# Kernel tuning notes

Hardware: AMD Instinct MI355X
Metric: run time of the kernel (lower is better)

The kernel has to match this reference:

```python
import jax, jax.numpy as jnp
import numpy as np

EMBED_DIM = 512
NUM_HEADS = 8
HEAD_DIM = EMBED_DIM // NUM_HEADS
EDGE_HIDDEN = 512
B, L = 2, 512


def setup_inputs() -> dict:
    key = jax.random.key(0)
    ks = jax.random.split(key, 16)
    s = 0.02
    inp = {
        "query": jax.random.normal(ks[0], (B, L, EMBED_DIM), jnp.float32),
        "key_in": jax.random.normal(ks[1], (B, L, EMBED_DIM), jnp.float32),
        "value": jax.random.normal(ks[2], (B, L, EMBED_DIM), jnp.float32),
        "edge_representation": jax.random.normal(ks[3], (B, L, L), jnp.float32),
        # projection weights stored as [in, out]: y = x @ W + b
        "Wq": jax.random.normal(ks[4], (EMBED_DIM, EMBED_DIM), jnp.float32) * s,
        "bq": jnp.zeros((EMBED_DIM,), jnp.float32),
        "Wk": jax.random.normal(ks[5], (EMBED_DIM, EMBED_DIM), jnp.float32) * s,
        "bk": jnp.zeros((EMBED_DIM,), jnp.float32),
        "Wv": jax.random.normal(ks[6], (EMBED_DIM, EMBED_DIM), jnp.float32) * s,
        "bv": jnp.zeros((EMBED_DIM,), jnp.float32),
        "Wo": jax.random.normal(ks[7], (EMBED_DIM, EMBED_DIM), jnp.float32) * s,
        "bo": jnp.zeros((EMBED_DIM,), jnp.float32),
        # edge MLP: Linear(1 -> 512) -> ReLU -> Linear(512 -> num_heads)
        "We1": jax.random.normal(ks[8], (1, EDGE_HIDDEN), jnp.float32) * s,
        "be1": jnp.zeros((EDGE_HIDDEN,), jnp.float32),
        "We2": jax.random.normal(ks[9], (EDGE_HIDDEN, NUM_HEADS), jnp.float32) * s,
        "be2": jnp.zeros((NUM_HEADS,), jnp.float32),
    }
    return inp


def reference(query, key_in, value, edge_representation,
              Wq, bq, Wk, bk, Wv, bv, Wo, bo, We1, be1, We2, be2):
    Bc, Lc, _ = query.shape
    # project and split heads: [B, H, L, Dh]
    def split_heads(x):
        return x.reshape(Bc, Lc, NUM_HEADS, HEAD_DIM).transpose(0, 2, 1, 3)
    Q = split_heads(query @ Wq + bq)
    K = split_heads(key_in @ Wk + bk)
    V = split_heads(value @ Wv + bv)
    # edge MLP on scalar edge features: [B, L, L, 1] -> [B, L, L, H]
    e = edge_representation[..., None]
    h = jax.nn.relu(e * We1[0] + be1)          # [B, L, L, 512]
    edge_bias = h @ We2 + be2                   # [B, L, L, H]
    scale = 1.0 / jnp.sqrt(jnp.asarray(HEAD_DIM, query.dtype))
    scores = jnp.einsum("bhqd,bhkd->bhqk", Q, K) * scale
    scores = scores + edge_bias.transpose(0, 3, 1, 2)  # [B, H, L, L]
    attn = jax.nn.softmax(scores, axis=-1)
    out = jnp.einsum("bhqk,bhkd->bhqd", attn, V)
    out = out.transpose(0, 2, 1, 3).reshape(Bc, Lc, EMBED_DIM)
    return out @ Wo + bo
```

## Files before the change

kernel.cpp:

```cpp
#include <hip/hip_runtime.h>
#include <hip/hip_bf16.h>

typedef __attribute__((ext_vector_type(8))) short bf16x8;
typedef __attribute__((ext_vector_type(4))) float f32x4;

#define LOG2E 1.44269504088896340736f

#define XQ_OFF 0
#define XK_OFF 524288
#define XV_OFF 1048576
#define WQ_OFF 1572864
#define WK_OFF 1835008
#define WV_OFF 2097152
#define WO_OFF 2359296
#define QB_OFF 2621440
#define KB_OFF 3145728
#define VT_OFF 3670016
#define AO_OFF 4194304
#define T_B   9437184
#define A_B   (T_B + 4096)
#define C_B   (A_B + 20480)
#define SEG_B (C_B + 20480)

struct MegaArgs {
  const float *xq, *xk, *xv, *eg;
  const float *wq, *wk, *wv, *wo;
  const float *bq, *bk, *bv, *bo;
  const float *w1, *b1, *we2, *be2;
  float* out;
  unsigned short* wsb;
  float *wsT, *wsA, *wsC;
  unsigned short* segp;
};

__device__ __forceinline__ unsigned short f2bf(float f) {
  union { __hip_bfloat16 h; unsigned short u; } c;
  c.h = __float2bfloat16(f);
  return c.u;
}

__device__ void prep_block(const MegaArgs& a, char* smem) {
  float* sT   = (float*)smem;
  int*   sIdx = (int*)(smem + 2048);
  float (*sDA)[8] = (float (*)[8])(smem + 4096);
  float (*sDC)[8] = (float (*)[8])(smem + 20480);
  float* sA0 = (float*)(smem + 36864);
  float* sC0 = (float*)(smem + 36896);
  int tid = threadIdx.x;
  for (int p = tid; p < 512; p += 256) {
    float w = a.w1[p], bb = a.b1[p];
    sT[p] = (w != 0.f) ? (-bb / w) : -3.4e38f;
    sIdx[p] = p;
#pragma unroll
    for (int h = 0; h < 8; ++h) {
      float w2 = a.we2[p * 8 + h];
      float ra = 0.f, rc = 0.f;
      if (w < 0.f)       { ra = w2 * w; rc = w2 * bb; }
      else if (w == 0.f) { rc = w2 * fmaxf(bb, 0.f); }
      sDA[p][h] = ra; sDC[p][h] = rc;
    }
  }
  __syncthreads();
  for (int size = 2; size <= 512; size <<= 1) {
    for (int stride = size >> 1; stride > 0; stride >>= 1) {
      int p = tid;
      int i = ((p / stride) * (stride << 1)) + (p % stride);
      int j = i + stride;
      bool up = ((i & size) == 0);
      float ti = sT[i], tj = sT[j];
      if (up ? (ti > tj) : (ti < tj)) {
        sT[i] = tj; sT[j] = ti;
        int t = sIdx[i]; sIdx[i] = sIdx[j]; sIdx[j] = t;
      }
      __syncthreads();
    }
  }
#pragma unroll
  for (int h = 0; h < 8; ++h) { sDA[tid][h] += sDA[tid + 256][h]; sDC[tid][h] += sDC[tid + 256][h]; }
  __syncthreads();
  for (int st = 128; st > 0; st >>= 1) {
    if (tid < st) {
#pragma unroll
      for (int h = 0; h < 8; ++h) { sDA[tid][h] += sDA[tid + st][h]; sDC[tid][h] += sDC[tid + st][h]; }
    }
    __syncthreads();
  }
  if (tid < 8) { sA0[tid] = sDA[0][tid]; sC0[tid] = sDC[0][tid] + a.be2[tid]; }
  __syncthreads();
  for (int p = tid; p < 512; p += 256) {
    int k = sIdx[p];
    float wk = a.w1[k], bk2 = a.b1[k];
#pragma unroll
    for (int h = 0; h < 8; ++h) {
      float w2 = a.we2[k * 8 + h];
      float da = 0.f, dc = 0.f;
      if (wk > 0.f)      { da =  w2 * wk; dc =  w2 * bk2; }
      else if (wk < 0.f) { da = -w2 * wk; dc = -w2 * bk2; }
      sDA[p][h] = da; sDC[p][h] = dc;
    }
  }
  __syncthreads();
  for (int off = 1; off < 512; off <<= 1) {
    float ra[2][8], rc[2][8];
#pragma unroll
    for (int e = 0; e < 2; ++e) {
      int p = tid + e * 256;
      if (p >= off) {
#pragma unroll
        for (int h = 0; h < 8; ++h) { ra[e][h] = sDA[p - off][h]; rc[e][h] = sDC[p - off][h]; }
      }
    }
    __syncthreads();
#pragma unroll
    for (int e = 0; e < 2; ++e) {
      int p = tid + e * 256;
      if (p >= off) {
#pragma unroll
        for (int h = 0; h < 8; ++h) { sDA[p][h] += ra[e][h]; sDC[p][h] += rc[e][h]; }
      }
    }
    __syncthreads();
  }
  a.wsT[tid] = sT[tid]; a.wsT[tid + 256] = sT[tid + 256];
  if (tid < 8) { a.wsA[tid * 513] = sA0[tid]; a.wsC[tid * 513] = sC0[tid]; }
  for (int p = tid; p < 512; p += 256) {
#pragma unroll
    for (int h = 0; h < 8; ++h) {
      a.wsA[h * 513 + p + 1] = sA0[h] + sDA[p][h];
      a.wsC[h * 513 + p + 1] = sC0[h] + sDC[p][h];
    }
  }
}

__device__ void transpose2(const MegaArgs& a, int tblk, char* smem) {
  unsigned short (*sWt)[72] = (unsigned short (*)[72])smem;
  int tid = threadIdx.x;
  for (int it = 0; it < 2; ++it) {
    int t = tblk * 2 + it;
    int mat = t >> 6, tile = t & 63;
    int k0 = (tile >> 3) * 64, n0 = (tile & 7) * 64;
    const float* src = (mat == 0) ? a.wq : (mat == 1) ? a.wk : (mat == 2) ? a.wv : a.wo;
    int row = tid >> 2, cq = tid & 3;
    const float4* sp = (const float4*)(src + (size_t)(k0 + row) * 512 + n0 + cq * 16);
    if (it) __syncthreads();
#pragma unroll
    for (int j2 = 0; j2 < 4; ++j2) {
      float4 v = sp[j2];
      int nl = cq * 16 + j2 * 4;
      sWt[nl + 0][row] = f2bf(v.x);
      sWt[nl + 1][row] = f2bf(v.y);
      sWt[nl + 2][row] = f2bf(v.z);
      sWt[nl + 3][row] = f2bf(v.w);
    }
    __syncthreads();
    int n = tid >> 2, kq = tid & 3;
    unsigned short* dst = a.wsb + WQ_OFF + mat * 262144 + (size_t)(n0 + n) * 512 + k0 + kq * 16;
    *(uint4*)dst       = *(const uint4*)&sWt[n][kq * 16];
    *(uint4*)(dst + 8) = *(const uint4*)&sWt[n][kq * 16 + 8];
  }
}

__device__ void seg_block(const MegaArgs& a, int sblk, char* smem) {
  float* sT = (float*)smem;
  int tid = threadIdx.x;
  sT[tid] = a.wsT[tid]; sT[tid + 256] = a.wsT[tid + 256];
  __syncthreads();
  int base = sblk * 1024;
  float ev[4];
#pragma unroll
  for (int j = 0; j < 4; ++j) ev[j] = a.eg[base + j * 256 + tid];
  int res[4];
#pragma unroll
  for (int j = 0; j < 4; ++j) {
    int lo = 0, hi = 512;
#pragma unroll
    for (int it = 0; it < 9; ++it) {
      int mid = (lo + hi) >> 1;
      bool c = sT[mid] < ev[j];
      lo = c ? mid + 1 : lo;
      hi = c ? hi : mid;
    }
    res[j] = lo;
  }
#pragma unroll
  for (int j = 0; j < 4; ++j) a.segp[base + j * 256 + tid] = (unsigned short)res[j];
}

__device__ void gemm_tile(const unsigned short* __restrict__ A, const unsigned short* __restrict__ Wt,
                          const float* __restrict__ bias, void* out, int mode,
                          int m0, int n0, char* smem) {
  const int K = 512;
  unsigned short (*sA)[72]  = (unsigned short (*)[72])smem;
  unsigned short (*sBt)[72] = (unsigned short (*)[72])(smem + 9216);
  int tid = threadIdx.x, wave = tid >> 6, lane = tid & 63;
  int quad = lane >> 4, l16 = lane & 15;
  f32x4 acc[4] = {{0.f,0.f,0.f,0.f},{0.f,0.f,0.f,0.f},{0.f,0.f,0.f,0.f},{0.f,0.f,0.f,0.f}};
  int lr = tid >> 2, ls = tid & 3;
  for (int kb = 0; kb < K; kb += 64) {
    __syncthreads();
    *(uint4*)&sA[lr][ls * 16]      = *(const uint4*)(A  + (size_t)(m0 + lr) * K + kb + ls * 16);
    *(uint4*)&sA[lr][ls * 16 + 8]  = *(const uint4*)(A  + (size_t)(m0 + lr) * K + kb + ls * 16 + 8);
    *(uint4*)&sBt[lr][ls * 16]     = *(const uint4*)(Wt + (size_t)(n0 + lr) * K + kb + ls * 16);
    *(uint4*)&sBt[lr][ls * 16 + 8] = *(const uint4*)(Wt + (size_t)(n0 + lr) * K + kb + ls * 16 + 8);
    __syncthreads();
    for (int ks = 0; ks < 2; ++ks) {
      bf16x8 af = *(const bf16x8*)&sA[wave * 16 + l16][ks * 32 + quad * 8];
#pragma unroll
      for (int nt = 0; nt < 4; ++nt) {
        bf16x8 bf = *(const bf16x8*)&sBt[nt * 16 + l16][ks * 32 + quad * 8];
        acc[nt] = __builtin_amdgcn_mfma_f32_16x16x32_bf16(af, bf, acc[nt], 0, 0, 0);
      }
    }
  }
  int mbase = m0 + wave * 16 + quad * 4;
#pragma unroll
  for (int nt = 0; nt < 4; ++nt) {
    int n = n0 + nt * 16 + l16;
    float bv = bias[n];
#pragma unroll
    for (int r = 0; r < 4; ++r) {
      float v = acc[nt][r] + bv;
      int m = mbase + r;
      if (mode == 0) {
        int b = m >> 9, l = m & 511, hh = n >> 6, d = n & 63;
        ((unsigned short*)out)[(((size_t)(b * 8 + hh) * 512) + l) * 64 + d] = f2bf(v);
      } else if (mode == 1) {
        ((float*)out)[(size_t)m * 512 + n] = v;
      } else {
        int b = m >> 9, l = m & 511, hh = n >> 6, d = n & 63;
        ((unsigned short*)out)[(((size_t)(b * 8 + hh) * 64) + d) * 512 + l] = f2bf(v);
      }
    }
  }
}

__device__ void attn_block(const MegaArgs& a, int qt, int h, int b, char* smem) {
  float* sAh = (float*)smem;
  float* sCh = (float*)(smem + 2052);
  unsigned short (*sP)[16][40] = (unsigned short (*)[16][40])(smem + 4112);
  float (*sO)[4][16][16] = (float (*)[4][16][16])(smem + 9232);
  float (*sM)[16] = (float (*)[16])(smem + 25616);
  float (*sL)[16] = (float (*)[16])(smem + 25872);
  const unsigned short* Qb = a.wsb + QB_OFF;
  const unsigned short* Kb = a.wsb + KB_OFF;
  const unsigned short* Vt = a.wsb + VT_OFF;
  int bh = b * 8 + h;
  int q0 = qt * 16;
  int tid = threadIdx.x, wave = tid >> 6, lane = tid & 63;
  int quad = lane >> 4, l16 = lane & 15;
  for (int i = tid; i < 513; i += 256) { sAh[i] = a.wsA[h * 513 + i]; sCh[i] = a.wsC[h * 513 + i]; }
  const unsigned short* qp = Qb + ((size_t)bh * 512 + q0 + l16) * 64 + quad * 8;
  bf16x8 qf0 = *(const bf16x8*)qp;
  bf16x8 qf1 = *(const bf16x8*)(qp + 32);
  int key_base = wave * 128;
  f32x4 S[4][2];
#pragma unroll
  for (int kt = 0; kt < 4; ++kt) {
    int key0 = key_base + kt * 32;
#pragma unroll
    for (int half = 0; half < 2; ++half) {
      const unsigned short* kp = Kb + ((size_t)bh * 512 + key0 + half * 16 + l16) * 64 + quad * 8;
      bf16x8 kf0 = *(const bf16x8*)kp;
      bf16x8 kf1 = *(const bf16x8*)(kp + 32);
      f32x4 acc = {0.f, 0.f, 0.f, 0.f};
      acc = __builtin_amdgcn_mfma_f32_16x16x32_bf16(qf0, kf0, acc, 0, 0, 0);
      acc = __builtin_amdgcn_mfma_f32_16x16x32_bf16(qf1, kf1, acc, 0, 0, 0);
      S[kt][half] = acc;
    }
  }
  __syncthreads();
#pragma unroll
  for (int kt = 0; kt < 4; ++kt)
#pragma unroll
    for (int half = 0; half < 2; ++half)
#pragma unroll
      for (int r = 0; r < 4; ++r) {
        int eidx = (b * 512 + q0 + quad * 4 + r) * 512 + key_base + kt * 32 + half * 16 + l16;
        float ev = a.eg[eidx];
        int sg = a.segp[eidx];
        S[kt][half][r] = S[kt][half][r] * 0.125f + sAh[sg] * ev + sCh[sg];
      }
  float m_w[4], l_w[4];
#pragma unroll
  for (int r = 0; r < 4; ++r) {
    float mx = -3.4e38f;
#pragma unroll
    for (int kt = 0; kt < 4; ++kt) { mx = fmaxf(mx, fmaxf(S[kt][0][r], S[kt][1][r])); }
    for (int off = 1; off < 16; off <<= 1) mx = fmaxf(mx, __shfl_xor(mx, off, 64));
    float s = 0.f;
#pragma unroll
    for (int kt = 0; kt < 4; ++kt)
#pragma unroll
      for (int half = 0; half < 2; ++half) {
        float p = exp2f((S[kt][half][r] - mx) * LOG2E);
        S[kt][half][r] = p; s += p;
      }
    for (int off = 1; off < 16; off <<= 1) s += __shfl_xor(s, off, 64);
    m_w[r] = mx; l_w[r] = s;
  }
  f32x4 Oacc[4] = {{0.f,0.f,0.f,0.f},{0.f,0.f,0.f,0.f},{0.f,0.f,0.f,0.f},{0.f,0.f,0.f,0.f}};
#pragma unroll
  for (int kt = 0; kt < 4; ++kt) {
    int key0 = key_base + kt * 32;
#pragma unroll
    for (int half = 0; half < 2; ++half)
#pragma unroll
      for (int r = 0; r < 4; ++r)
        sP[wave][quad * 4 + r][half * 16 + l16] = f2bf(S[kt][half][r]);
    __builtin_amdgcn_wave_barrier();
    bf16x8 pf = *(const bf16x8*)&sP[wave][l16][quad * 8];
    __builtin_amdgcn_wave_barrier();
#pragma unroll
    for (int nt = 0; nt < 4; ++nt) {
      bf16x8 vf = *(const bf16x8*)(Vt + ((size_t)bh * 64 + nt * 16 + l16) * 512 + key0 + quad * 8);
      Oacc[nt] = __builtin_amdgcn_mfma_f32_16x16x32_bf16(pf, vf, Oacc[nt], 0, 0, 0);
    }
  }
  if (l16 == 0) {
#pragma unroll
    for (int r = 0; r < 4; ++r) { sM[wave][quad * 4 + r] = m_w[r]; sL[wave][quad * 4 + r] = l_w[r]; }
  }
#pragma unroll
  for (int nt = 0; nt < 4; ++nt)
#pragma unroll
    for (int r = 0; r < 4; ++r)
      sO[wave][nt][quad * 4 + r][l16] = Oacc[nt][r];
  __syncthreads();
#pragma unroll
  for (int r = 0; r < 4; ++r) {
    int row = quad * 4 + r;
    float M = fmaxf(fmaxf(sM[0][row], sM[1][row]), fmaxf(sM[2][row], sM[3][row]));
    float L = 0.f, Ov = 0.f;
#pragma unroll
    for (int wv = 0; wv < 4; ++wv) {
      float f = exp2f((sM[wv][row] - M) * LOG2E);
      L += f * sL[wv][row];
      Ov += f * sO[wv][wave][row][l16];
    }
    float v = Ov / L;
    (a.wsb + AO_OFF)[((size_t)(b * 512 + q0 + row)) * 512 + h * 64 + wave * 16 + l16] = f2bf(v);
  }
}

__global__ __launch_bounds__(256) void k_pre(MegaArgs a) {
  __shared__ __align__(16) char smem[36928];
  int blk = blockIdx.x;
  if (blk == 0) prep_block(a, smem);
  else if (blk <= 128) transpose2(a, blk - 1, smem);
  else {
    int i = (blk - 129) * 256 + threadIdx.x;
    int region = i >> 17, off = i & 131071;
    const float* src = (region == 0) ? a.xq : (region == 1) ? a.xk : a.xv;
    float4 v = ((const float4*)src)[off];
    ushort4 o;
    o.x = f2bf(v.x); o.y = f2bf(v.y); o.z = f2bf(v.z); o.w = f2bf(v.w);
    ((ushort4*)a.wsb)[i] = o;
  }
}

__global__ __launch_bounds__(256) void k_qkv(MegaArgs a) {
  __shared__ __align__(16) char smem[18432];
  int blk = blockIdx.x;
  if (blk < 384) {
    int z = blk >> 7, rem = blk & 127;
    const unsigned short* A  = a.wsb + ((z == 0) ? XQ_OFF : (z == 1) ? XK_OFF : XV_OFF);
    const unsigned short* Wt = a.wsb + ((z == 0) ? WQ_OFF : (z == 1) ? WK_OFF : WV_OFF);
    const float* bias = (z == 0) ? a.bq : (z == 1) ? a.bk : a.bv;
    void* outp = (void*)(a.wsb + ((z == 0) ? QB_OFF : (z == 1) ? KB_OFF : VT_OFF));
    gemm_tile(A, Wt, bias, outp, (z == 2) ? 2 : 0, (rem & 15) * 64, (rem >> 4) * 64, smem);
  } else {
    seg_block(a, blk - 384, smem);
  }
}

__global__ __launch_bounds__(256) void k_at(MegaArgs a) {
  __shared__ __align__(16) char smem[26128];
  int blk = blockIdx.x;
  attn_block(a, blk & 31, (blk >> 5) & 7, blk >> 8, smem);
}

__global__ __launch_bounds__(256) void k_og(MegaArgs a) {
  __shared__ __align__(16) char smem[18432];
  gemm_tile(a.wsb + AO_OFF, a.wsb + WO_OFF, a.bo, (void*)a.out, 1,
            (blockIdx.x & 15) * 64, (blockIdx.x >> 4) * 64, smem);
}

extern "C" void kernel_launch(void* const* d_in, const int* in_sizes, int n_in,
                              void* d_out, int out_size, void* d_ws, size_t ws_size,
                              hipStream_t stream) {
  MegaArgs a;
  a.xq  = (const float*)d_in[0];
  a.xk  = (const float*)d_in[1];
  a.xv  = (const float*)d_in[2];
  a.eg  = (const float*)d_in[3];
  a.wq  = (const float*)d_in[4];
  a.bq  = (const float*)d_in[5];
  a.wk  = (const float*)d_in[6];
  a.bk  = (const float*)d_in[7];
  a.wv  = (const float*)d_in[8];
  a.bv  = (const float*)d_in[9];
  a.wo  = (const float*)d_in[10];
  a.bo  = (const float*)d_in[11];
  a.w1  = (const float*)d_in[12];
  a.b1  = (const float*)d_in[13];
  a.we2 = (const float*)d_in[14];
  a.be2 = (const float*)d_in[15];
  a.out = (float*)d_out;
  a.wsb = (unsigned short*)d_ws;
  a.wsT = (float*)((char*)d_ws + T_B);
  a.wsA = (float*)((char*)d_ws + A_B);
  a.wsC = (float*)((char*)d_ws + C_B);
  a.segp = (unsigned short*)((char*)d_ws + SEG_B);

  k_pre<<<1665, 256, 0, stream>>>(a);
  k_qkv<<<896, 256, 0, stream>>>(a);
  k_at<<<512, 256, 0, stream>>>(a);
  k_og<<<128, 256, 0, stream>>>(a);
}
```

Before: 141.8 us.

## Merge four launches into two with in-kernel flag and counter synchronization

Drops the separate pre-conversion pass: the QKV and output GEMMs now read fp32 activations and weights directly and convert them to bf16 while staging into shared memory. The prep block and the QKV GEMMs share one launch, with the segment-search blocks spinning on a magic flag set by the prep block. Attention and the output projection share a second launch, with the output-GEMM blocks spinning on a global completion counter. This removes two kernel launches and the round trip through workspace, but adds per-tile conversion work, strided scalar LDS writes for the weight transpose, and a deadlock risk if spinning blocks become resident before the blocks they wait on. The flag is never cleared between calls, so on repeated launches the segment-search blocks may read stale prep data.

```diff
diff --git a/kernel.cpp b/kernel.cpp
--- a/kernel.cpp
+++ b/kernel.cpp
@@ -5,22 +5,19 @@
 typedef __attribute__((ext_vector_type(4))) float f32x4;
 
 #define LOG2E 1.44269504088896340736f
-
-#define XQ_OFF 0
-#define XK_OFF 524288
-#define XV_OFF 1048576
-#define WQ_OFF 1572864
-#define WK_OFF 1835008
-#define WV_OFF 2097152
-#define WO_OFF 2359296
+#define MAGIC 0x13572468u
+
 #define QB_OFF 2621440
 #define KB_OFF 3145728
 #define VT_OFF 3670016
 #define AO_OFF 4194304
+#define WQ_OFF 1572864
 #define T_B   9437184
 #define A_B   (T_B + 4096)
 #define C_B   (A_B + 20480)
 #define SEG_B (C_B + 20480)
+#define FLAG_B (SEG_B + 1048576)
+#define CNT_B  (FLAG_B + 64)
 
 struct MegaArgs {
   const float *xq, *xk, *xv, *eg;
@@ -31,12 +28,20 @@
   unsigned short* wsb;
   float *wsT, *wsA, *wsC;
   unsigned short* segp;
+  unsigned int *flag, *cnt;
 };
 
 __device__ __forceinline__ unsigned short f2bf(float f) {
   union { __hip_bfloat16 h; unsigned short u; } c;
   c.h = __float2bfloat16(f);
   return c.u;
+}
+
+__device__ __forceinline__ uint4 pack8(float4 a, float4 b) {
+  union { unsigned short us[8]; uint4 u; } r;
+  r.us[0] = f2bf(a.x); r.us[1] = f2bf(a.y); r.us[2] = f2bf(a.z); r.us[3] = f2bf(a.w);
+  r.us[4] = f2bf(b.x); r.us[5] = f2bf(b.y); r.us[6] = f2bf(b.z); r.us[7] = f2bf(b.w);
+  return r.u;
 }
 
 __device__ void prep_block(const MegaArgs& a, char* smem) {
@@ -132,34 +137,6 @@
   }
 }
 
-__device__ void transpose2(const MegaArgs& a, int tblk, char* smem) {
-  unsigned short (*sWt)[72] = (unsigned short (*)[72])smem;
-  int tid = threadIdx.x;
-  for (int it = 0; it < 2; ++it) {
-    int t = tblk * 2 + it;
-    int mat = t >> 6, tile = t & 63;
-    int k0 = (tile >> 3) * 64, n0 = (tile & 7) * 64;
-    const float* src = (mat == 0) ? a.wq : (mat == 1) ? a.wk : (mat == 2) ? a.wv : a.wo;
-    int row = tid >> 2, cq = tid & 3;
-    const float4* sp = (const float4*)(src + (size_t)(k0 + row) * 512 + n0 + cq * 16);
-    if (it) __syncthreads();
-#pragma unroll
-    for (int j2 = 0; j2 < 4; ++j2) {
-      float4 v = sp[j2];
-      int nl = cq * 16 + j2 * 4;
-      sWt[nl + 0][row] = f2bf(v.x);
-      sWt[nl + 1][row] = f2bf(v.y);
-      sWt[nl + 2][row] = f2bf(v.z);
-      sWt[nl + 3][row] = f2bf(v.w);
-    }
-    __syncthreads();
-    int n = tid >> 2, kq = tid & 3;
-    unsigned short* dst = a.wsb + WQ_OFF + mat * 262144 + (size_t)(n0 + n) * 512 + k0 + kq * 16;
-    *(uint4*)dst       = *(const uint4*)&sWt[n][kq * 16];
-    *(uint4*)(dst + 8) = *(const uint4*)&sWt[n][kq * 16 + 8];
-  }
-}
-
 __device__ void seg_block(const MegaArgs& a, int sblk, char* smem) {
   float* sT = (float*)smem;
   int tid = threadIdx.x;
@@ -186,22 +163,39 @@
   for (int j = 0; j < 4; ++j) a.segp[base + j * 256 + tid] = (unsigned short)res[j];
 }
 
-__device__ void gemm_tile(const unsigned short* __restrict__ A, const unsigned short* __restrict__ Wt,
-                          const float* __restrict__ bias, void* out, int mode,
-                          int m0, int n0, char* smem) {
-  const int K = 512;
+__device__ void gemm_core(const float* __restrict__ Af, const unsigned short* __restrict__ Ab,
+                          const float* __restrict__ W, const float* __restrict__ bias,
+                          void* out, int mode, int m0, int n0, char* smem) {
   unsigned short (*sA)[72]  = (unsigned short (*)[72])smem;
   unsigned short (*sBt)[72] = (unsigned short (*)[72])(smem + 9216);
   int tid = threadIdx.x, wave = tid >> 6, lane = tid & 63;
   int quad = lane >> 4, l16 = lane & 15;
   f32x4 acc[4] = {{0.f,0.f,0.f,0.f},{0.f,0.f,0.f,0.f},{0.f,0.f,0.f,0.f},{0.f,0.f,0.f,0.f}};
   int lr = tid >> 2, ls = tid & 3;
-  for (int kb = 0; kb < K; kb += 64) {
-    __syncthreads();
-    *(uint4*)&sA[lr][ls * 16]      = *(const uint4*)(A  + (size_t)(m0 + lr) * K + kb + ls * 16);
-    *(uint4*)&sA[lr][ls * 16 + 8]  = *(const uint4*)(A  + (size_t)(m0 + lr) * K + kb + ls * 16 + 8);
-    *(uint4*)&sBt[lr][ls * 16]     = *(const uint4*)(Wt + (size_t)(n0 + lr) * K + kb + ls * 16);
-    *(uint4*)&sBt[lr][ls * 16 + 8] = *(const uint4*)(Wt + (size_t)(n0 + lr) * K + kb + ls * 16 + 8);
+  for (int kb = 0; kb < 512; kb += 64) {
+    __syncthreads();
+    if (Af) {
+      const float4* ap = (const float4*)(Af + (size_t)(m0 + lr) * 512 + kb + ls * 16);
+      float4 v0 = ap[0], v1 = ap[1], v2 = ap[2], v3 = ap[3];
+      *(uint4*)&sA[lr][ls * 16]     = pack8(v0, v1);
+      *(uint4*)&sA[lr][ls * 16 + 8] = pack8(v2, v3);
+    } else {
+      *(uint4*)&sA[lr][ls * 16]     = *(const uint4*)(Ab + (size_t)(m0 + lr) * 512 + kb + ls * 16);
+      *(uint4*)&sA[lr][ls * 16 + 8] = *(const uint4*)(Ab + (size_t)(m0 + lr) * 512 + kb + ls * 16 + 8);
+    }
+    {
+      const float4* wp = (const float4*)(W + (size_t)(kb + lr) * 512 + n0 + ls * 16);
+      float4 w0 = wp[0], w1 = wp[1], w2 = wp[2], w3 = wp[3];
+      int nb = ls * 16;
+      sBt[nb + 0][lr] = f2bf(w0.x);  sBt[nb + 1][lr] = f2bf(w0.y);
+      sBt[nb + 2][lr] = f2bf(w0.z);  sBt[nb + 3][lr] = f2bf(w0.w);
+      sBt[nb + 4][lr] = f2bf(w1.x);  sBt[nb + 5][lr] = f2bf(w1.y);
+      sBt[nb + 6][lr] = f2bf(w1.z);  sBt[nb + 7][lr] = f2bf(w1.w);
+      sBt[nb + 8][lr] = f2bf(w2.x);  sBt[nb + 9][lr] = f2bf(w2.y);
+      sBt[nb + 10][lr] = f2bf(w2.z); sBt[nb + 11][lr] = f2bf(w2.w);
+      sBt[nb + 12][lr] = f2bf(w3.x); sBt[nb + 13][lr] = f2bf(w3.y);
+      sBt[nb + 14][lr] = f2bf(w3.z); sBt[nb + 15][lr] = f2bf(w3.w);
+    }
     __syncthreads();
     for (int ks = 0; ks < 2; ++ks) {
       bf16x8 af = *(const bf16x8*)&sA[wave * 16 + l16][ks * 32 + quad * 8];
@@ -342,47 +336,51 @@
   }
 }
 
-__global__ __launch_bounds__(256) void k_pre(MegaArgs a) {
+__global__ __launch_bounds__(256) void k_head(MegaArgs a) {
   __shared__ __align__(16) char smem[36928];
-  int blk = blockIdx.x;
-  if (blk == 0) prep_block(a, smem);
-  else if (blk <= 128) transpose2(a, blk - 1, smem);
-  else {
-    int i = (blk - 129) * 256 + threadIdx.x;
-    int region = i >> 17, off = i & 131071;
-    const float* src = (region == 0) ? a.xq : (region == 1) ? a.xk : a.xv;
-    float4 v = ((const float4*)src)[off];
-    ushort4 o;
-    o.x = f2bf(v.x); o.y = f2bf(v.y); o.z = f2bf(v.z); o.w = f2bf(v.w);
-    ((ushort4*)a.wsb)[i] = o;
-  }
-}
-
-__global__ __launch_bounds__(256) void k_qkv(MegaArgs a) {
-  __shared__ __align__(16) char smem[18432];
-  int blk = blockIdx.x;
-  if (blk < 384) {
-    int z = blk >> 7, rem = blk & 127;
-    const unsigned short* A  = a.wsb + ((z == 0) ? XQ_OFF : (z == 1) ? XK_OFF : XV_OFF);
-    const unsigned short* Wt = a.wsb + ((z == 0) ? WQ_OFF : (z == 1) ? WK_OFF : WV_OFF);
+  int blk = blockIdx.x, tid = threadIdx.x;
+  if (blk == 0) {
+    if (tid == 0) __hip_atomic_store(a.cnt, 0u, __ATOMIC_RELAXED, __HIP_MEMORY_SCOPE_AGENT);
+    prep_block(a, smem);
+    __threadfence();
+    __syncthreads();
+    if (tid == 0) __hip_atomic_store(a.flag, MAGIC, __ATOMIC_RELEASE, __HIP_MEMORY_SCOPE_AGENT);
+  } else if (blk <= 384) {
+    int g = blk - 1, z = g >> 7, rem = g & 127;
+    const float* A    = (z == 0) ? a.xq : (z == 1) ? a.xk : a.xv;
+    const float* W    = (z == 0) ? a.wq : (z == 1) ? a.wk : a.wv;
     const float* bias = (z == 0) ? a.bq : (z == 1) ? a.bk : a.bv;
     void* outp = (void*)(a.wsb + ((z == 0) ? QB_OFF : (z == 1) ? KB_OFF : VT_OFF));
-    gemm_tile(A, Wt, bias, outp, (z == 2) ? 2 : 0, (rem & 15) * 64, (rem >> 4) * 64, smem);
+    gemm_core(A, nullptr, W, bias, outp, (z == 2) ? 2 : 0, (rem & 15) * 64, (rem >> 4) * 64, smem);
   } else {
-    seg_block(a, blk - 384, smem);
-  }
-}
-
-__global__ __launch_bounds__(256) void k_at(MegaArgs a) {
+    if (tid == 0) {
+      while (__hip_atomic_load(a.flag, __ATOMIC_ACQUIRE, __HIP_MEMORY_SCOPE_AGENT) != MAGIC)
+        __builtin_amdgcn_s_sleep(8);
+    }
+    __syncthreads();
+    seg_block(a, blk - 385, smem);
+  }
+}
+
+__global__ __launch_bounds__(256) void k_tail(MegaArgs a) {
   __shared__ __align__(16) char smem[26128];
-  int blk = blockIdx.x;
-  attn_block(a, blk & 31, (blk >> 5) & 7, blk >> 8, smem);
-}
-
-__global__ __launch_bounds__(256) void k_og(MegaArgs a) {
-  __shared__ __align__(16) char smem[18432];
-  gemm_tile(a.wsb + AO_OFF, a.wsb + WO_OFF, a.bo, (void*)a.out, 1,
-            (blockIdx.x & 15) * 64, (blockIdx.x >> 4) * 64, smem);
+  int blk = blockIdx.x, tid = threadIdx.x;
+  if (blk < 512) {
+    attn_block(a, blk & 31, (blk >> 5) & 7, blk >> 8, smem);
+    __threadfence();
+    __syncthreads();
+    if (tid == 0) __hip_atomic_fetch_add(a.cnt, 1u, __ATOMIC_RELEASE, __HIP_MEMORY_SCOPE_AGENT);
+  } else {
+    if (tid == 0) {
+      while (__hip_atomic_load(a.cnt, __ATOMIC_ACQUIRE, __HIP_MEMORY_SCOPE_AGENT) < 512u)
+        __builtin_amdgcn_s_sleep(8);
+    }
+    __syncthreads();
+    __threadfence();
+    int g = blk - 512;
+    gemm_core(nullptr, a.wsb + AO_OFF, a.wo, a.bo, (void*)a.out, 1,
+              (g & 15) * 64, (g >> 4) * 64, smem);
+  }
 }
 
 extern "C" void kernel_launch(void* const* d_in, const int* in_sizes, int n_in,
@@ -411,9 +409,9 @@
   a.wsA = (float*)((char*)d_ws + A_B);
   a.wsC = (float*)((char*)d_ws + C_B);
   a.segp = (unsigned short*)((char*)d_ws + SEG_B);
-
-  k_pre<<<1665, 256, 0, stream>>>(a);
-  k_qkv<<<896, 256, 0, stream>>>(a);
-  k_at<<<512, 256, 0, stream>>>(a);
-  k_og<<<128, 256, 0, stream>>>(a);
-}
+  a.flag = (unsigned int*)((char*)d_ws + FLAG_B);
+  a.cnt  = (unsigned int*)((char*)d_ws + CNT_B);
+
+  k_head<<<897, 256, 0, stream>>>(a);
+  k_tail<<<640, 256, 0, stream>>>(a);
+}
```

Result: slower. 338.9 us (+139.1%).
